# Performance work log

Measured on AMD Instinct MI355X. Metric: run time of the kernel, lower is better.

Reference implementation:

```python
import jax, jax.numpy as jnp
import numpy as np


def _binarize_kernel_wise(w):
    # Bi-ViT LinearBi (Qmodes.kernel_wise): per-output-channel scale alpha = mean(|w|)
    # quantized weight w_q = alpha * sign(w).  w: [out, in]
    alpha = jnp.mean(jnp.abs(w), axis=1, keepdims=True)  # [out, 1]
    return alpha * jnp.sign(w)


def setup_inputs() -> dict:
    key = jax.random.key(0)
    k_x, k_w1, k_b1, k_w2, k_b2 = jax.random.split(key, 5)
    B, N, C, H = 64, 197, 768, 3072
    x = jax.random.normal(k_x, (B, N, C), dtype=jnp.float32)
    w1 = jax.random.normal(k_w1, (H, C), dtype=jnp.float32) * 0.02
    b1 = jax.random.normal(k_b1, (H,), dtype=jnp.float32) * 0.02
    w2 = jax.random.normal(k_w2, (C, H), dtype=jnp.float32) * 0.02
    b2 = jax.random.normal(k_b2, (C,), dtype=jnp.float32) * 0.02
    return {"x": x, "w1": w1, "b1": b1, "w2": w2, "b2": b2}


def reference(x, w1, b1, w2, b2):
    # fc1 (binarized linear, kernel-wise scales)
    w1_q = _binarize_kernel_wise(w1)
    h = jnp.einsum('bnc,hc->bnh', x, w1_q) + b1
    # GELU (exact, erf-based as torch nn.GELU default) then clip to [-10, 10]
    h = jnp.clip(jax.nn.gelu(h, approximate=False), -10.0, 10.0)
    # dropout p=0.0 -> identity
    w2_q = _binarize_kernel_wise(w2)
    out = jnp.einsum('bnh,ch->bnc', h, w2_q) + b2
    return out
```

## Files before the change

kernel.cpp:

```cpp
#include <hip/hip_runtime.h>
#include <hip/hip_bf16.h>
#include <cstdint>
#include <cstddef>


typedef __bf16 bf16x8 __attribute__((ext_vector_type(8)));
typedef __bf16 bf16x4 __attribute__((ext_vector_type(4)));
typedef float floatx4 __attribute__((ext_vector_type(4)));

__device__ __forceinline__ void async_load16(const void* g, void* l) {
    __builtin_amdgcn_global_load_lds(
        (const __attribute__((address_space(1))) void*)g,
        (__attribute__((address_space(3))) void*)l,
        16, 0, 0);
}

__global__ __launch_bounds__(256) void prep_all(
    const float* __restrict__ x,
    const float* __restrict__ w1,
    const float* __restrict__ w2,
    __hip_bfloat16* __restrict__ xb,
    __hip_bfloat16* __restrict__ sgn1, float* __restrict__ alpha1,
    __hip_bfloat16* __restrict__ sgn2, float* __restrict__ alpha2,
    int ncvt)
{
    const int b = blockIdx.x;
    if (b < ncvt) {
        const int i = b * 256 + threadIdx.x;
        float4 v = ((const float4*)x)[i];
        bf16x4 o;
        o[0] = (__bf16)v.x; o[1] = (__bf16)v.y;
        o[2] = (__bf16)v.z; o[3] = (__bf16)v.w;
        ((bf16x4*)xb)[i] = o;
        return;
    }
    const float* w; __hip_bfloat16* sgn; float* alpha; int cols4; int row;
    if (b < ncvt + 3072) {
        w = w1; sgn = sgn1; alpha = alpha1; cols4 = 192; row = b - ncvt;
    } else {
        w = w2; sgn = sgn2; alpha = alpha2; cols4 = 768; row = b - ncvt - 3072;
    }
    const float4* wr = (const float4*)w + (size_t)row * cols4;
    bf16x4* sr = (bf16x4*)sgn + (size_t)row * cols4;
    float s = 0.0f;
    for (int c = threadIdx.x; c < cols4; c += 256) {
        float4 v = wr[c];
        s += fabsf(v.x) + fabsf(v.y) + fabsf(v.z) + fabsf(v.w);
        bf16x4 o;
        o[0] = (__bf16)(v.x > 0.0f ? 1.0f : (v.x < 0.0f ? -1.0f : 0.0f));
        o[1] = (__bf16)(v.y > 0.0f ? 1.0f : (v.y < 0.0f ? -1.0f : 0.0f));
        o[2] = (__bf16)(v.z > 0.0f ? 1.0f : (v.z < 0.0f ? -1.0f : 0.0f));
        o[3] = (__bf16)(v.w > 0.0f ? 1.0f : (v.w < 0.0f ? -1.0f : 0.0f));
        sr[c] = o;
    }
    #pragma unroll
    for (int off = 32; off > 0; off >>= 1) s += __shfl_down(s, off, 64);
    __shared__ float wsum[4];
    const int lane = threadIdx.x & 63;
    const int wv = threadIdx.x >> 6;
    if (lane == 0) wsum[wv] = s;
    __syncthreads();
    if (threadIdx.x == 0) {
        float t = wsum[0] + wsum[1] + wsum[2] + wsum[3];
        alpha[row] = t / (float)(cols4 * 4);
    }
}

__device__ __forceinline__ void store_val(__hip_bfloat16* C, size_t idx, float v) {
    C[idx] = __float2bfloat16(v);
}
__device__ __forceinline__ void store_val(float* C, size_t idx, float v) {
    C[idx] = v;
}

template <bool DO_GELU, typename OutT>
__global__ __launch_bounds__(256) void gemm_bin(
    const __hip_bfloat16* __restrict__ A,
    const __hip_bfloat16* __restrict__ S,
    const float* __restrict__ alpha,
    const float* __restrict__ bias,
    OutT* __restrict__ C,
    int M, int N, int K, int T, int perXcd)
{
    constexpr int TM = 128;
    constexpr int TN = 128;
    constexpr int TK = 64;

    const int b = blockIdx.x;
    const int l = (b & 7) * perXcd + (b >> 3);
    if (l >= T) return;
    const int NT = N / TN;
    const int mt = l / NT;
    const int nt = l - mt * NT;
    const int bm = mt * TM;
    const int bn = nt * TN;

    __shared__ __align__(16) __hip_bfloat16 sA[TM * TK];
    __shared__ __align__(16) __hip_bfloat16 sB[TN * TK];

    const int tid = threadIdx.x;
    const int wave = tid >> 6;
    const int lane = tid & 63;

    const int wm = (wave & 1) * 64;
    const int wn = (wave >> 1) * 64;
    const int lr = lane & 15;
    const int kq = lane >> 4;
    const int e3 = lr & 7;

    const int crow = lane >> 3;
    const int ccol = ((lane & 7) ^ crow) * 8;

    floatx4 acc[4][4];
    #pragma unroll
    for (int i = 0; i < 4; i++)
        #pragma unroll
        for (int j = 0; j < 4; j++)
            #pragma unroll
            for (int r = 0; r < 4; r++)
                acc[i][j][r] = 0.0f;

    for (int k0 = 0; k0 < K; k0 += TK) {
        #pragma unroll
        for (int t = 0; t < 8; t++) {
            const int seg = wave * 8 + t;
            if (seg < 16) {
                const int r = seg * 8 + crow;
                int ar = bm + r;
                ar = ar < M ? ar : (M - 1);
                async_load16(A + (size_t)ar * K + (k0 + ccol), (void*)(sA + seg * 512));
            } else {
                const int r = (seg - 16) * 8 + crow;
                async_load16(S + (size_t)(bn + r) * K + (k0 + ccol),
                             (void*)(sB + (seg - 16) * 512));
            }
        }
        __syncthreads();

        #pragma unroll
        for (int ks = 0; ks < 2; ks++) {
            const int slot = ((ks << 2) | kq) ^ e3;
            bf16x8 af[4], bfv[4];
            #pragma unroll
            for (int i = 0; i < 4; i++)
                af[i] = *(const bf16x8*)(sA + (wm + i * 16 + lr) * TK + slot * 8);
            #pragma unroll
            for (int j = 0; j < 4; j++)
                bfv[j] = *(const bf16x8*)(sB + (wn + j * 16 + lr) * TK + slot * 8);
            #pragma unroll
            for (int i = 0; i < 4; i++)
                #pragma unroll
                for (int j = 0; j < 4; j++)
                    acc[i][j] = __builtin_amdgcn_mfma_f32_16x16x32_bf16(
                        af[i], bfv[j], acc[i][j], 0, 0, 0);
        }
        __syncthreads();
    }

    float al[4], bi[4];
    #pragma unroll
    for (int j = 0; j < 4; j++) {
        const int col = bn + wn + j * 16 + lr;
        al[j] = alpha[col];
        bi[j] = bias[col];
    }
    #pragma unroll
    for (int i = 0; i < 4; i++) {
        const int row0 = bm + wm + i * 16 + kq * 4;
        #pragma unroll
        for (int r = 0; r < 4; r++) {
            const int row = row0 + r;
            if (row < M) {
                #pragma unroll
                for (int j = 0; j < 4; j++) {
                    float v = acc[i][j][r] * al[j] + bi[j];
                    if (DO_GELU) {
                        v = 0.5f * v * (1.0f + erff(v * 0.70710678118654752f));
                        v = fminf(fmaxf(v, -10.0f), 10.0f);
                    }
                    store_val(C, (size_t)row * N + (bn + wn + j * 16 + lr), v);
                }
            }
        }
    }
}

extern "C" void kernel_launch(void* const* d_in, const int* in_sizes, int n_in,
                              void* d_out, int out_size, void* d_ws, size_t ws_size,
                              hipStream_t stream) {
    const float* x  = (const float*)d_in[0];
    const float* w1 = (const float*)d_in[1];
    const float* b1 = (const float*)d_in[2];
    const float* w2 = (const float*)d_in[3];
    const float* b2 = (const float*)d_in[4];

    const int M = 64 * 197;
    const int Cd = 768;
    const int Hd = 3072;

    char* ws = (char*)d_ws;
    __hip_bfloat16* xb   = (__hip_bfloat16*)ws;
    __hip_bfloat16* sgn1 = xb + (size_t)M * Cd;
    __hip_bfloat16* sgn2 = sgn1 + (size_t)Hd * Cd;
    float* alpha1 = (float*)(sgn2 + (size_t)Cd * Hd);
    float* alpha2 = alpha1 + Hd;
    __hip_bfloat16* hbuf = (__hip_bfloat16*)(alpha2 + Cd);

    const int ncvt = (M * Cd) / 4 / 256;
    prep_all<<<ncvt + Hd + Cd, 256, 0, stream>>>(
        x, w1, w2, xb, sgn1, alpha1, sgn2, alpha2, ncvt);

    const int gm = (M + 127) / 128;

    {
        const int T = (Hd / 128) * gm;
        const int perXcd = (T + 7) / 8;
        gemm_bin<true, __hip_bfloat16><<<perXcd * 8, 256, 0, stream>>>(
            xb, sgn1, alpha1, b1, hbuf, M, Hd, Cd, T, perXcd);
    }
    {
        const int T = (Cd / 128) * gm;
        const int perXcd = (T + 7) / 8;
        gemm_bin<false, float><<<perXcd * 8, 256, 0, stream>>>(
            hbuf, sgn2, alpha2, b2, (float*)d_out, M, Cd, Hd, T, perXcd);
    }
}
```

Baseline: 264.6 us.

## Rewrite GEMM as 256x256 tile, 8-wave, double-buffered LDS pipeline

Both binarized GEMMs now use 256x256 output tiles with 512 threads, 128 KB of dynamic LDS double-buffered across K steps, and a four-phase schedule. Each phase interleaves LDS fragment reads, async global-to-LDS prefetch of the next tiles, and MFMA bursts raised with s_setprio. The XCD tile mapping is recomputed for an exact grid. The aim is more reuse per tile and hiding global load latency behind compute. In exchange it uses many more registers and LDS, occupancy is limited, and the second GEMM gets only 3 column tiles, so there are fewer blocks to fill the GPU.

Result: slower. 296.1 us (+11.9%).

```diff
diff --git a/kernel.cpp b/kernel.cpp
--- a/kernel.cpp
+++ b/kernel.cpp
@@ -74,111 +74,201 @@
 }
 
 template <bool DO_GELU, typename OutT>
-__global__ __launch_bounds__(256) void gemm_bin(
+__global__ __launch_bounds__(512, 2) void gemm_bin(
     const __hip_bfloat16* __restrict__ A,
     const __hip_bfloat16* __restrict__ S,
     const float* __restrict__ alpha,
     const float* __restrict__ bias,
     OutT* __restrict__ C,
-    int M, int N, int K, int T, int perXcd)
+    int M, int N, int K, int T)
 {
-    constexpr int TM = 128;
-    constexpr int TN = 128;
-    constexpr int TK = 64;
+    extern __shared__ __align__(16) __hip_bfloat16 lds[];
 
     const int b = blockIdx.x;
-    const int l = (b & 7) * perXcd + (b >> 3);
+    const int xcd = b & 7, rest = b >> 3;
+    const int q8 = T >> 3, r8 = T & 7;
+    const int l = (xcd < r8 ? xcd * (q8 + 1) : r8 * (q8 + 1) + (xcd - r8) * q8) + rest;
     if (l >= T) return;
-    const int NT = N / TN;
-    const int mt = l / NT;
-    const int nt = l - mt * NT;
-    const int bm = mt * TM;
-    const int bn = nt * TN;
-
-    __shared__ __align__(16) __hip_bfloat16 sA[TM * TK];
-    __shared__ __align__(16) __hip_bfloat16 sB[TN * TK];
+    const int NTL = N >> 8;
+    const int mt = l / NTL;
+    const int nt = l - mt * NTL;
+    const int bm = mt << 8;
+    const int bn = nt << 8;
 
     const int tid = threadIdx.x;
-    const int wave = tid >> 6;
+    const int w = tid >> 6;
     const int lane = tid & 63;
-
-    const int wm = (wave & 1) * 64;
-    const int wn = (wave >> 1) * 64;
+    const int wm = w & 1;
+    const int wn = w >> 1;
     const int lr = lane & 15;
     const int kq = lane >> 4;
     const int e3 = lr & 7;
-
     const int crow = lane >> 3;
-    const int ccol = ((lane & 7) ^ crow) * 8;
-
-    floatx4 acc[4][4];
+    const int ccol = ((lane & 7) ^ crow) << 3;
+
+    const int NT = K >> 6;
+
+    const int idx0 = w << 1;
+    const int sALo0 = (w < 4) ? idx0 : idx0 + 8;
+    const int sAHi0 = sALo0 + 8;
+    const int sBLo0 = (w >> 1) * 8 + (w & 1) * 2;
+    const int sBHi0 = sBLo0 + 4;
+
+    const int aoff  = (wm * 128 + lr) * 64;
+    const int boff0 = (wn * 64 + lr) * 64;
+    const int k0off = (kq ^ e3) * 8;
+    const int k1off = k0off ^ 32;
+
+    floatx4 acc[8][4];
     #pragma unroll
-    for (int i = 0; i < 4; i++)
+    for (int i = 0; i < 8; ++i)
         #pragma unroll
-        for (int j = 0; j < 4; j++)
+        for (int j = 0; j < 4; ++j)
             #pragma unroll
-            for (int r = 0; r < 4; r++)
-                acc[i][j][r] = 0.0f;
-
-    for (int k0 = 0; k0 < K; k0 += TK) {
-        #pragma unroll
-        for (int t = 0; t < 8; t++) {
-            const int seg = wave * 8 + t;
-            if (seg < 16) {
-                const int r = seg * 8 + crow;
-                int ar = bm + r;
-                ar = ar < M ? ar : (M - 1);
-                async_load16(A + (size_t)ar * K + (k0 + ccol), (void*)(sA + seg * 512));
-            } else {
-                const int r = (seg - 16) * 8 + crow;
-                async_load16(S + (size_t)(bn + r) * K + (k0 + ccol),
-                             (void*)(sB + (seg - 16) * 512));
-            }
+            for (int r = 0; r < 4; ++r) acc[i][j][r] = 0.0f;
+
+    bf16x8 aH[4][2];
+    bf16x8 bF[4][2];
+
+#define STA(dst, k0_, seg) do {                                             \
+    int r_ = bm + (seg) * 8 + crow; r_ = r_ < M ? r_ : M - 1;               \
+    async_load16(A + (size_t)r_ * K + ((k0_) + ccol),                       \
+                 (void*)((dst) + (seg) * 512));                             \
+} while (0)
+#define STB(dst, k0_, seg) do {                                             \
+    const int r_ = bn + (seg) * 8 + crow;                                   \
+    async_load16(S + (size_t)r_ * K + ((k0_) + ccol),                       \
+                 (void*)((dst) + (seg) * 512));                             \
+} while (0)
+#define LDA4(hbase)                                                         \
+    _Pragma("unroll")                                                       \
+    for (int a2 = 0; a2 < 4; ++a2) {                                        \
+        const __hip_bfloat16* pa_ = bufA + aoff + ((hbase) + a2) * 1024;    \
+        aH[a2][0] = *(const bf16x8*)(pa_ + k0off);                          \
+        aH[a2][1] = *(const bf16x8*)(pa_ + k1off);                          \
+    }
+#define LDB2(bcbase)                                                        \
+    _Pragma("unroll")                                                       \
+    for (int b2 = 0; b2 < 2; ++b2) {                                        \
+        const __hip_bfloat16* pb_ = bufB + boff0 + ((bcbase) + b2) * 1024;  \
+        bF[(bcbase) + b2][0] = *(const bf16x8*)(pb_ + k0off);               \
+        bF[(bcbase) + b2][1] = *(const bf16x8*)(pb_ + k1off);               \
+    }
+#define MM8(arb, bcb)                                                       \
+    _Pragma("unroll")                                                       \
+    for (int a2 = 0; a2 < 4; ++a2) {                                        \
+        _Pragma("unroll")                                                   \
+        for (int b2 = 0; b2 < 2; ++b2) {                                    \
+            acc[(arb) + a2][(bcb) + b2] =                                   \
+                __builtin_amdgcn_mfma_f32_16x16x32_bf16(                    \
+                    aH[a2][0], bF[(bcb) + b2][0],                           \
+                    acc[(arb) + a2][(bcb) + b2], 0, 0, 0);                  \
+            acc[(arb) + a2][(bcb) + b2] =                                   \
+                __builtin_amdgcn_mfma_f32_16x16x32_bf16(                    \
+                    aH[a2][1], bF[(bcb) + b2][1],                           \
+                    acc[(arb) + a2][(bcb) + b2], 0, 0, 0);                  \
+        }                                                                   \
+    }
+
+    {
+        __hip_bfloat16* a0 = lds;
+        __hip_bfloat16* b0 = lds + 16384;
+        STA(a0, 0, sALo0); STA(a0, 0, sALo0 + 1);
+        STB(b0, 0, sBLo0); STB(b0, 0, sBLo0 + 1);
+        STA(a0, 0, sAHi0); STA(a0, 0, sAHi0 + 1);
+        STB(b0, 0, sBHi0); STB(b0, 0, sBHi0 + 1);
+        __hip_bfloat16* a1 = lds + 32768;
+        __hip_bfloat16* b1 = lds + 49152;
+        STA(a1, 64, sALo0); STA(a1, 64, sALo0 + 1);
+        STB(b1, 64, sBLo0); STB(b1, 64, sBLo0 + 1);
+        STA(a1, 64, sAHi0); STA(a1, 64, sAHi0 + 1);
+        asm volatile("s_waitcnt vmcnt(6)" ::: "memory");
+        __builtin_amdgcn_sched_barrier(0);
+        __builtin_amdgcn_s_barrier();
+    }
+
+    for (int i = 0; i < NT; ++i) {
+        const int p = i & 1;
+        __hip_bfloat16* bufA = lds + p * 32768;
+        __hip_bfloat16* bufB = bufA + 16384;
+        __hip_bfloat16* othB = lds + (p ^ 1) * 32768 + 16384;
+        const int kn1 = (i + 1) << 6;
+        const int kn2 = (i + 2) << 6;
+        const bool s1 = (i + 1) < NT;
+        const bool s2 = (i + 2) < NT;
+
+        LDA4(0);
+        LDB2(0);
+        if (s1) { STB(othB, kn1, sBHi0); STB(othB, kn1, sBHi0 + 1); }
+        __builtin_amdgcn_s_barrier();
+        asm volatile("s_waitcnt lgkmcnt(0)" ::: "memory");
+        __builtin_amdgcn_sched_barrier(0);
+        __builtin_amdgcn_s_setprio(1);
+        MM8(0, 0);
+        __builtin_amdgcn_s_setprio(0);
+        __builtin_amdgcn_s_barrier();
+
+        LDB2(2);
+        if (s2) { STA(bufA, kn2, sALo0); STA(bufA, kn2, sALo0 + 1); }
+        __builtin_amdgcn_s_barrier();
+        asm volatile("s_waitcnt lgkmcnt(0)" ::: "memory");
+        __builtin_amdgcn_sched_barrier(0);
+        __builtin_amdgcn_s_setprio(1);
+        MM8(0, 2);
+        __builtin_amdgcn_s_setprio(0);
+        __builtin_amdgcn_s_barrier();
+
+        LDA4(4);
+        if (s2) { STB(bufB, kn2, sBLo0); STB(bufB, kn2, sBLo0 + 1); }
+        __builtin_amdgcn_s_barrier();
+        asm volatile("s_waitcnt lgkmcnt(0)" ::: "memory");
+        __builtin_amdgcn_sched_barrier(0);
+        __builtin_amdgcn_s_setprio(1);
+        MM8(4, 2);
+        __builtin_amdgcn_s_setprio(0);
+        __builtin_amdgcn_s_barrier();
+
+        if (s2) { STA(bufA, kn2, sAHi0); STA(bufA, kn2, sAHi0 + 1); }
+        if (s1) {
+            if (s2) asm volatile("s_waitcnt vmcnt(6)" ::: "memory");
+            else    asm volatile("s_waitcnt vmcnt(0)" ::: "memory");
+            __builtin_amdgcn_sched_barrier(0);
         }
-        __syncthreads();
-
-        #pragma unroll
-        for (int ks = 0; ks < 2; ks++) {
-            const int slot = ((ks << 2) | kq) ^ e3;
-            bf16x8 af[4], bfv[4];
-            #pragma unroll
-            for (int i = 0; i < 4; i++)
-                af[i] = *(const bf16x8*)(sA + (wm + i * 16 + lr) * TK + slot * 8);
-            #pragma unroll
-            for (int j = 0; j < 4; j++)
-                bfv[j] = *(const bf16x8*)(sB + (wn + j * 16 + lr) * TK + slot * 8);
-            #pragma unroll
-            for (int i = 0; i < 4; i++)
-                #pragma unroll
-                for (int j = 0; j < 4; j++)
-                    acc[i][j] = __builtin_amdgcn_mfma_f32_16x16x32_bf16(
-                        af[i], bfv[j], acc[i][j], 0, 0, 0);
-        }
-        __syncthreads();
-    }
+        __builtin_amdgcn_s_barrier();
+        __builtin_amdgcn_s_setprio(1);
+        MM8(4, 0);
+        __builtin_amdgcn_s_setprio(0);
+        __builtin_amdgcn_s_barrier();
+    }
+
+#undef STA
+#undef STB
+#undef LDA4
+#undef LDB2
+#undef MM8
 
     float al[4], bi[4];
     #pragma unroll
-    for (int j = 0; j < 4; j++) {
-        const int col = bn + wn + j * 16 + lr;
-        al[j] = alpha[col];
-        bi[j] = bias[col];
+    for (int bc = 0; bc < 4; ++bc) {
+        const int col = bn + wn * 64 + bc * 16 + lr;
+        al[bc] = alpha[col];
+        bi[bc] = bias[col];
     }
     #pragma unroll
-    for (int i = 0; i < 4; i++) {
-        const int row0 = bm + wm + i * 16 + kq * 4;
+    for (int ar = 0; ar < 8; ++ar) {
+        const int row0 = bm + wm * 128 + ar * 16 + kq * 4;
         #pragma unroll
-        for (int r = 0; r < 4; r++) {
+        for (int r = 0; r < 4; ++r) {
             const int row = row0 + r;
             if (row < M) {
                 #pragma unroll
-                for (int j = 0; j < 4; j++) {
-                    float v = acc[i][j][r] * al[j] + bi[j];
+                for (int bc = 0; bc < 4; ++bc) {
+                    float v = acc[ar][bc][r] * al[bc] + bi[bc];
                     if (DO_GELU) {
                         v = 0.5f * v * (1.0f + erff(v * 0.70710678118654752f));
                         v = fminf(fmaxf(v, -10.0f), 10.0f);
                     }
-                    store_val(C, (size_t)row * N + (bn + wn + j * 16 + lr), v);
+                    store_val(C, (size_t)row * N + (bn + wn * 64 + bc * 16 + lr), v);
                 }
             }
         }
@@ -210,18 +300,22 @@
     prep_all<<<ncvt + Hd + Cd, 256, 0, stream>>>(
         x, w1, w2, xb, sgn1, alpha1, sgn2, alpha2, ncvt);
 
-    const int gm = (M + 127) / 128;
+    const int gm = (M + 255) / 256;
 
     {
-        const int T = (Hd / 128) * gm;
-        const int perXcd = (T + 7) / 8;
-        gemm_bin<true, __hip_bfloat16><<<perXcd * 8, 256, 0, stream>>>(
-            xb, sgn1, alpha1, b1, hbuf, M, Hd, Cd, T, perXcd);
+        const int T = (Hd / 256) * gm;
+        hipFuncSetAttribute(
+            reinterpret_cast<const void*>(&gemm_bin<true, __hip_bfloat16>),
+            hipFuncAttributeMaxDynamicSharedMemorySize, 131072);
+        gemm_bin<true, __hip_bfloat16><<<T, 512, 131072, stream>>>(
+            xb, sgn1, alpha1, b1, hbuf, M, Hd, Cd, T);
     }
     {
-        const int T = (Cd / 128) * gm;
-        const int perXcd = (T + 7) / 8;
-        gemm_bin<false, float><<<perXcd * 8, 256, 0, stream>>>(
-            hbuf, sgn2, alpha2, b2, (float*)d_out, M, Cd, Hd, T, perXcd);
-    }
-}
+        const int T = (Cd / 256) * gm;
+        hipFuncSetAttribute(
+            reinterpret_cast<const void*>(&gemm_bin<false, float>),
+            hipFuncAttributeMaxDynamicSharedMemorySize, 131072);
+        gemm_bin<false, float><<<T, 512, 131072, stream>>>(
+            hbuf, sgn2, alpha2, b2, (float*)d_out, M, Cd, Hd, T);
+    }
+}
```

## Add 8-wave 128x256 double-buffered pipelined GEMM kernel for fc1

Applied to the files above, without the earlier changes.

The first GEMM now runs in a new 512-thread kernel with 128x256 tiles and double-buffered dynamic LDS (96KB). Global-to-LDS async loads for later K-steps are interleaved with four MFMA quadrant phases, using explicit waitcnt, barriers and setprio to overlap memory with compute. It also changes the XCD block remapping to handle tile counts that are not a multiple of 8. The aim is to hide load latency and raise MFMA utilisation in the larger GEMM, at the cost of more LDS, more registers per thread and fragile hand-tuned synchronisation. The second GEMM keeps the old kernel under a new name.

Result: slower. 278.3 us (+5.2%).

```diff
diff --git a/kernel.cpp b/kernel.cpp
--- a/kernel.cpp
+++ b/kernel.cpp
@@ -74,7 +74,208 @@
 }
 
 template <bool DO_GELU, typename OutT>
-__global__ __launch_bounds__(256) void gemm_bin(
+__global__ __launch_bounds__(512, 2) void gemm_bin_8w(
+    const __hip_bfloat16* __restrict__ A,
+    const __hip_bfloat16* __restrict__ S,
+    const float* __restrict__ alpha,
+    const float* __restrict__ bias,
+    OutT* __restrict__ C,
+    int M, int N, int K, int T)
+{
+    extern __shared__ __align__(16) __hip_bfloat16 lds[];
+
+    const int b = blockIdx.x;
+    const int xcd = b & 7, rest = b >> 3;
+    const int q8 = T >> 3, r8 = T & 7;
+    const int l = (xcd < r8 ? xcd * (q8 + 1) : r8 * (q8 + 1) + (xcd - r8) * q8) + rest;
+    if (l >= T) return;
+    const int NTL = N >> 8;
+    const int mt = l / NTL;
+    const int nt = l - mt * NTL;
+    const int bm = mt << 7;
+    const int bn = nt << 8;
+
+    const int tid = threadIdx.x;
+    const int w = tid >> 6;
+    const int lane = tid & 63;
+    const int wm = w & 1;
+    const int wn = w >> 1;
+    const int lr = lane & 15;
+    const int kq = lane >> 4;
+    const int e3 = lr & 7;
+    const int crow = lane >> 3;
+    const int ccol = ((lane & 7) ^ crow) << 3;
+
+    const int NT = K >> 6;
+
+    const int sALo = ((w >> 2) << 3) + (w & 3);
+    const int sAHi = sALo + 4;
+    const int sBLo = ((w >> 1) << 3) + ((w & 1) << 1);
+    const int sBHi = sBLo + 4;
+
+    const int k0off = (kq ^ e3) * 8;
+    const int k1off = k0off ^ 32;
+
+    floatx4 acc[4][4];
+    #pragma unroll
+    for (int i = 0; i < 4; ++i)
+        #pragma unroll
+        for (int j = 0; j < 4; ++j)
+            #pragma unroll
+            for (int r = 0; r < 4; ++r) acc[i][j][r] = 0.0f;
+
+    bf16x8 aF[4][2];
+    bf16x8 bF[4][2];
+
+#define STA(dst, k0_, seg) do {                                             \
+    int r_ = bm + (seg) * 8 + crow; r_ = r_ < M ? r_ : M - 1;               \
+    async_load16(A + (size_t)r_ * K + ((k0_) + ccol),                       \
+                 (void*)((dst) + (seg) * 512));                             \
+} while (0)
+#define STB(dst, k0_, seg) do {                                             \
+    const int r_ = bn + (seg) * 8 + crow;                                   \
+    async_load16(S + (size_t)r_ * K + ((k0_) + ccol),                       \
+                 (void*)((dst) + (seg) * 512));                             \
+} while (0)
+#define LDA2(rtb)                                                           \
+    _Pragma("unroll")                                                       \
+    for (int a2 = 0; a2 < 2; ++a2) {                                        \
+        const __hip_bfloat16* pa_ =                                         \
+            bufA + (wm * 64 + ((rtb) + a2) * 16 + lr) * 64;                 \
+        aF[(rtb) + a2][0] = *(const bf16x8*)(pa_ + k0off);                  \
+        aF[(rtb) + a2][1] = *(const bf16x8*)(pa_ + k1off);                  \
+    }
+#define LDB2(ctb)                                                           \
+    _Pragma("unroll")                                                       \
+    for (int b2 = 0; b2 < 2; ++b2) {                                        \
+        const __hip_bfloat16* pb_ =                                         \
+            bufB + (wn * 64 + ((ctb) + b2) * 16 + lr) * 64;                 \
+        bF[(ctb) + b2][0] = *(const bf16x8*)(pb_ + k0off);                  \
+        bF[(ctb) + b2][1] = *(const bf16x8*)(pb_ + k1off);                  \
+    }
+#define MMQ(rtb, ctb)                                                       \
+    _Pragma("unroll")                                                       \
+    for (int a2 = 0; a2 < 2; ++a2) {                                        \
+        _Pragma("unroll")                                                   \
+        for (int b2 = 0; b2 < 2; ++b2) {                                    \
+            acc[(rtb) + a2][(ctb) + b2] =                                   \
+                __builtin_amdgcn_mfma_f32_16x16x32_bf16(                    \
+                    aF[(rtb) + a2][0], bF[(ctb) + b2][0],                   \
+                    acc[(rtb) + a2][(ctb) + b2], 0, 0, 0);                  \
+            acc[(rtb) + a2][(ctb) + b2] =                                   \
+                __builtin_amdgcn_mfma_f32_16x16x32_bf16(                    \
+                    aF[(rtb) + a2][1], bF[(ctb) + b2][1],                   \
+                    acc[(rtb) + a2][(ctb) + b2], 0, 0, 0);                  \
+        }                                                                   \
+    }
+
+    {
+        __hip_bfloat16* a0 = lds;
+        __hip_bfloat16* b0 = lds + 16384;
+        STA(a0, 0, sALo);
+        STB(b0, 0, sBLo); STB(b0, 0, sBLo + 1);
+        STA(a0, 0, sAHi);
+        STB(b0, 0, sBHi); STB(b0, 0, sBHi + 1);
+        __hip_bfloat16* a1 = lds + 8192;
+        __hip_bfloat16* b1 = lds + 32768;
+        STA(a1, 64, sALo);
+        STB(b1, 64, sBLo); STB(b1, 64, sBLo + 1);
+        STA(a1, 64, sAHi);
+        asm volatile("s_waitcnt vmcnt(4)" ::: "memory");
+        __builtin_amdgcn_sched_barrier(0);
+        __builtin_amdgcn_s_barrier();
+    }
+
+    for (int i = 0; i < NT; ++i) {
+        const int p = i & 1;
+        __hip_bfloat16* bufA = lds + p * 8192;
+        __hip_bfloat16* bufB = lds + 16384 + p * 16384;
+        __hip_bfloat16* othB = lds + 16384 + (p ^ 1) * 16384;
+        const int kn1 = (i + 1) << 6;
+        const int kn2 = (i + 2) << 6;
+        const bool s1 = (i + 1) < NT;
+        const bool s2 = (i + 2) < NT;
+
+        LDA2(0);
+        LDB2(0);
+        if (s1) { STB(othB, kn1, sBHi); STB(othB, kn1, sBHi + 1); }
+        __builtin_amdgcn_s_barrier();
+        asm volatile("s_waitcnt lgkmcnt(0)" ::: "memory");
+        __builtin_amdgcn_sched_barrier(0);
+        __builtin_amdgcn_s_setprio(1);
+        MMQ(0, 0);
+        __builtin_amdgcn_s_setprio(0);
+        __builtin_amdgcn_s_barrier();
+
+        LDB2(2);
+        if (s2) STA(bufA, kn2, sALo);
+        __builtin_amdgcn_s_barrier();
+        asm volatile("s_waitcnt lgkmcnt(0)" ::: "memory");
+        __builtin_amdgcn_sched_barrier(0);
+        __builtin_amdgcn_s_setprio(1);
+        MMQ(0, 2);
+        __builtin_amdgcn_s_setprio(0);
+        __builtin_amdgcn_s_barrier();
+
+        LDA2(2);
+        if (s2) { STB(bufB, kn2, sBLo); STB(bufB, kn2, sBLo + 1); }
+        __builtin_amdgcn_s_barrier();
+        asm volatile("s_waitcnt lgkmcnt(0)" ::: "memory");
+        __builtin_amdgcn_sched_barrier(0);
+        __builtin_amdgcn_s_setprio(1);
+        MMQ(2, 2);
+        __builtin_amdgcn_s_setprio(0);
+        __builtin_amdgcn_s_barrier();
+
+        if (s2) STA(bufA, kn2, sAHi);
+        if (s1) {
+            if (s2) asm volatile("s_waitcnt vmcnt(4)" ::: "memory");
+            else    asm volatile("s_waitcnt vmcnt(0)" ::: "memory");
+            __builtin_amdgcn_sched_barrier(0);
+        }
+        __builtin_amdgcn_s_barrier();
+        __builtin_amdgcn_s_setprio(1);
+        MMQ(2, 0);
+        __builtin_amdgcn_s_setprio(0);
+        __builtin_amdgcn_s_barrier();
+    }
+
+#undef STA
+#undef STB
+#undef LDA2
+#undef LDB2
+#undef MMQ
+
+    float al[4], bi[4];
+    #pragma unroll
+    for (int bc = 0; bc < 4; ++bc) {
+        const int col = bn + wn * 64 + bc * 16 + lr;
+        al[bc] = alpha[col];
+        bi[bc] = bias[col];
+    }
+    #pragma unroll
+    for (int ar = 0; ar < 4; ++ar) {
+        const int row0 = bm + wm * 64 + ar * 16 + kq * 4;
+        #pragma unroll
+        for (int r = 0; r < 4; ++r) {
+            const int row = row0 + r;
+            if (row < M) {
+                #pragma unroll
+                for (int bc = 0; bc < 4; ++bc) {
+                    float v = acc[ar][bc][r] * al[bc] + bi[bc];
+                    if (DO_GELU) {
+                        v = 0.5f * v * (1.0f + erff(v * 0.70710678118654752f));
+                        v = fminf(fmaxf(v, -10.0f), 10.0f);
+                    }
+                    store_val(C, (size_t)row * N + (bn + wn * 64 + bc * 16 + lr), v);
+                }
+            }
+        }
+    }
+}
+
+template <bool DO_GELU, typename OutT>
+__global__ __launch_bounds__(256) void gemm_bin_128(
     const __hip_bfloat16* __restrict__ A,
     const __hip_bfloat16* __restrict__ S,
     const float* __restrict__ alpha,
@@ -213,15 +414,17 @@
     const int gm = (M + 127) / 128;
 
     {
-        const int T = (Hd / 128) * gm;
-        const int perXcd = (T + 7) / 8;
-        gemm_bin<true, __hip_bfloat16><<<perXcd * 8, 256, 0, stream>>>(
-            xb, sgn1, alpha1, b1, hbuf, M, Hd, Cd, T, perXcd);
+        const int T = (Hd / 256) * gm;
+        hipFuncSetAttribute(
+            reinterpret_cast<const void*>(&gemm_bin_8w<true, __hip_bfloat16>),
+            hipFuncAttributeMaxDynamicSharedMemorySize, 98304);
+        gemm_bin_8w<true, __hip_bfloat16><<<T, 512, 98304, stream>>>(
+            xb, sgn1, alpha1, b1, hbuf, M, Hd, Cd, T);
     }
     {
         const int T = (Cd / 128) * gm;
         const int perXcd = (T + 7) / 8;
-        gemm_bin<false, float><<<perXcd * 8, 256, 0, stream>>>(
+        gemm_bin_128<false, float><<<perXcd * 8, 256, 0, stream>>>(
             hbuf, sgn2, alpha2, b2, (float*)d_out, M, Cd, Hd, T, perXcd);
     }
 }
```
